# Performance work log

Hardware: AMD Instinct MI355X
Metric: run time of the kernel (lower is better)

## Reference

```python
import jax, jax.numpy as jnp
import numpy as np

H, QP, VP, D, DP = 4, 4, 4, 128, 64
DH = D // H


def setup_inputs() -> dict:
    key = jax.random.key(0)
    ks = jax.random.split(key, 16)
    B, L = 1, 1024
    w_c0 = float(np.log(np.e - 1.0))
    inp = {
        'single': jax.random.normal(ks[0], (B, L, D), jnp.float32),
        'pair': jax.random.normal(ks[1], (B, L, L, DP), jnp.float32),
        'T': jax.random.normal(ks[2], (B, L, 4, 4), jnp.float32),
        'w_C': jnp.full((H,), w_c0, jnp.float32),
        'ln_g': jnp.ones((D,), jnp.float32),
        'ln_b': jnp.zeros((D,), jnp.float32),
        'Wq': jax.random.normal(ks[3], (D, H * DH), jnp.float32) * 0.05,
        'Wk': jax.random.normal(ks[4], (D, H * DH), jnp.float32) * 0.05,
        'Wv': jax.random.normal(ks[5], (D, H * DH), jnp.float32) * 0.05,
        'Wqpt': jax.random.normal(ks[6], (D, H * QP * 3), jnp.float32) * 0.05,
        'Wkpt': jax.random.normal(ks[7], (D, H * QP * 3), jnp.float32) * 0.05,
        'Wvpt': jax.random.normal(ks[8], (D, H * VP * 3), jnp.float32) * 0.05,
        'Wb': jax.random.normal(ks[9], (DP, H), jnp.float32) * 0.05,
        'Wout': jax.random.normal(ks[10], (H * (DH + DP + VP * 3 + VP), D), jnp.float32) * 0.05,
        'b_out': jnp.zeros((D,), jnp.float32),
    }
    return inp


def _layernorm(x, g, b, eps=1e-5):
    x32 = x.astype(jnp.float32)
    mu = x32.mean(-1, keepdims=True)
    var = ((x32 - mu) ** 2).mean(-1, keepdims=True)
    return ((x32 - mu) * jax.lax.rsqrt(var + eps) * g + b).astype(x.dtype)


def reference(single, pair, T, w_C, ln_g, ln_b, Wq, Wk, Wv, Wqpt, Wkpt, Wvpt, Wb, Wout, b_out):
    B, L, Dm = single.shape
    scale_attn = DH ** (-0.5)
    z = _layernorm(single, ln_g, ln_b)
    Q = (z @ Wq).reshape(B, L, H, DH)
    K = (z @ Wk).reshape(B, L, H, DH)
    V = (z @ Wv).reshape(B, L, H, DH)
    Q_pt = (z @ Wqpt).reshape(B, L, H, QP, 3)
    K_pt = (z @ Wkpt).reshape(B, L, H, QP, 3)
    V_pt = (z @ Wvpt).reshape(B, L, H, VP, 3)
    R = T[..., :3, :3]   # [B,L,3,3]
    t = T[..., :3, 3]    # [B,L,3]
    # global-frame points: R @ p + t
    Q_g = jnp.einsum('blxy,blhpy->blhpx', R, Q_pt) + t[:, :, None, None, :]
    K_g = jnp.einsum('blxy,blhpy->blhpx', R, K_pt) + t[:, :, None, None, :]
    V_g = jnp.einsum('blxy,blhpy->blhpx', R, V_pt) + t[:, :, None, None, :]
    # scalar QK score [B,H,L,L]
    s_attn = jnp.einsum('bihd,bjhd->bhij', Q, K) * scale_attn
    # pair bias [B,H,L,L]
    b_attn = jnp.einsum('bijc,ch->bhij', pair, Wb)
    # squared point distance [B,H,L,L]
    diff = Q_g[:, :, None] - K_g[:, None]          # [B,L,L,H,QP,3]
    d2 = jnp.moveaxis((diff ** 2).sum((-1, -2)), -1, 1)
    w_pt = jax.nn.softplus(w_C)[None, :, None, None]
    attn = jax.nn.softmax(s_attn + b_attn - 0.5 * w_pt * d2, axis=-1)
    # scalar values [B,L,H*DH]
    o_s = jnp.einsum('bhij,bjhd->bihd', attn, V).reshape(B, L, H * DH)
    # point values aggregated in global frame then mapped back: R^T (p - t)
    o_pt_g = jnp.einsum('bhij,bjhpx->bihpx', attn, V_g)
    o_pt = jnp.einsum('blyx,blhpy->blhpx', R, o_pt_g - t[:, :, None, None, :])
    o_pt_n = jnp.sqrt((o_pt ** 2).sum(-1))
    # pair aggregation [B,L,H*DP]
    o_pair = jnp.einsum('bhij,bijc->bihc', attn, pair).reshape(B, L, H * DP)
    out = jnp.concatenate([o_s, o_pair, o_pt.reshape(B, L, -1), o_pt_n.reshape(B, L, -1)], axis=-1)
    return single + out @ Wout + b_out
```

## Files before the change

kernel.cpp:

```cpp
#include <hip/hip_runtime.h>
#include <math.h>

#define L_SEQ 1024
#define DM 128
#define JC 32
#define NCH (L_SEQ / JC)

#define OFF_KHAT 0
#define OFF_QHAT (L_SEQ * 192)
#define OFF_V    (OFF_QHAT + L_SEQ * 192)
#define OFF_VG   (OFF_V + L_SEQ * DM)

typedef __attribute__((address_space(1))) const void* gas_t;
typedef __attribute__((address_space(3))) void* las_t;

__device__ __forceinline__ void async16(const float4* g, float4* l) {
    __builtin_amdgcn_global_load_lds((gas_t)g, (las_t)l, 16, 0, 0);
}
#define ASYNC_BAR() asm volatile("s_waitcnt lgkmcnt(0)\n\ts_barrier" ::: "memory")

__global__ __launch_bounds__(256) void ipa_prep(
    const float* __restrict__ single, const float* __restrict__ T,
    const float* __restrict__ w_C, const float* __restrict__ ln_g, const float* __restrict__ ln_b,
    const float* __restrict__ Wq, const float* __restrict__ Wk, const float* __restrict__ Wv,
    const float* __restrict__ Wqpt, const float* __restrict__ Wkpt, const float* __restrict__ Wvpt,
    float* __restrict__ ws)
{
    __shared__ float z_lds[4][128];
    __shared__ float proj[4][528];
    __shared__ float qg[4][4][4][3];
    __shared__ float kg[4][4][4][3];
    __shared__ float cq[4][4], ck[4][4];

    const int t = threadIdx.x;
    const int wv = t >> 6, lane = t & 63;
    const int i0 = blockIdx.x << 2;
    const int i = i0 + wv;

    float x0 = single[i*DM + lane];
    float x1 = single[i*DM + 64 + lane];
    float s = x0 + x1, s2 = x0*x0 + x1*x1;
    #pragma unroll
    for (int off = 1; off < 64; off <<= 1) { s += __shfl_xor(s, off); s2 += __shfl_xor(s2, off); }
    float mu = s * 0.0078125f;
    float var = s2 * 0.0078125f - mu*mu;
    float rs = rsqrtf(var + 1e-5f);
    z_lds[wv][lane]      = (x0 - mu) * rs * ln_g[lane]      + ln_b[lane];
    z_lds[wv][lane + 64] = (x1 - mu) * rs * ln_g[lane + 64] + ln_b[lane + 64];
    __syncthreads();

    for (int cc = t; cc < 528; cc += 256) {
        const float* W; int col, ncol;
        if (cc < 128)      { W = Wq;   col = cc;       ncol = 128; }
        else if (cc < 256) { W = Wk;   col = cc - 128; ncol = 128; }
        else if (cc < 384) { W = Wv;   col = cc - 256; ncol = 128; }
        else if (cc < 432) { W = Wqpt; col = cc - 384; ncol = 48;  }
        else if (cc < 480) { W = Wkpt; col = cc - 432; ncol = 48;  }
        else               { W = Wvpt; col = cc - 480; ncol = 48;  }
        float a0 = 0.f, a1 = 0.f, a2 = 0.f, a3 = 0.f;
        #pragma unroll 8
        for (int k = 0; k < 128; ++k) {
            float w = W[k*ncol + col];
            a0 = fmaf(z_lds[0][k], w, a0);
            a1 = fmaf(z_lds[1][k], w, a1);
            a2 = fmaf(z_lds[2][k], w, a2);
            a3 = fmaf(z_lds[3][k], w, a3);
        }
        proj[0][cc] = a0; proj[1][cc] = a1; proj[2][cc] = a2; proj[3][cc] = a3;
    }
    __syncthreads();

    if (t < 64) {
        int r = t >> 4, h = (t >> 2) & 3, p = t & 3;
        int ii = i0 + r;
        float R[3][3], tt[3];
        #pragma unroll
        for (int x = 0; x < 3; ++x) {
            #pragma unroll
            for (int y = 0; y < 3; ++y) R[x][y] = T[ii*16 + x*4 + y];
            tt[x] = T[ii*16 + x*4 + 3];
        }
        int base = 384 + (h*4 + p)*3;
        float q0 = proj[r][base],    q1 = proj[r][base+1],  q2 = proj[r][base+2];
        float k0 = proj[r][base+48], k1 = proj[r][base+49], k2 = proj[r][base+50];
        float v0 = proj[r][base+96], v1 = proj[r][base+97], v2 = proj[r][base+98];
        #pragma unroll
        for (int x = 0; x < 3; ++x) {
            float qq = R[x][0]*q0 + R[x][1]*q1 + R[x][2]*q2 + tt[x];
            float kk = R[x][0]*k0 + R[x][1]*k1 + R[x][2]*k2 + tt[x];
            float vv = R[x][0]*v0 + R[x][1]*v1 + R[x][2]*v2 + tt[x];
            qg[r][h][p][x] = qq;
            kg[r][h][p][x] = kk;
            ws[OFF_VG + ii*48 + h*12 + p*3 + x] = vv;
        }
    }
    __syncthreads();

    if (t < 32) {
        int r = t >> 3, h = (t >> 1) & 3, isk = t & 1;
        float w = w_C[h];
        float wp = log1pf(__expf(w));
        float sq = 0.f;
        #pragma unroll
        for (int p = 0; p < 4; ++p)
            #pragma unroll
            for (int x = 0; x < 3; ++x) {
                float g = isk ? kg[r][h][p][x] : qg[r][h][p][x];
                sq += g*g;
            }
        float c = -0.5f * wp * sq;
        if (isk) ck[r][h] = c; else cq[r][h] = c;
    }
    __syncthreads();

    for (int idx = t; idx < 512; idx += 256) {
        int r = idx >> 7, d = idx & 127;
        ws[OFF_V + (size_t)(i0 + r)*DM + d] = proj[r][256 + d];
    }
    const float scale_attn = 0.17677669529663687f;
    for (int idx = t; idx < 768; idx += 256) {
        int r = idx / 192, rem = idx % 192;
        int h = rem / 48, k = rem % 48;
        int ii = i0 + r;
        float w = w_C[h];
        float wp = log1pf(__expf(w));
        float kv, qv;
        if (k < 32) {
            kv = proj[r][128 + h*32 + k];
            qv = scale_attn * proj[r][h*32 + k];
        } else if (k < 44) {
            int e = k - 32;
            kv = kg[r][h][e/3][e%3];
            qv = wp * qg[r][h][e/3][e%3];
        } else if (k == 44) { kv = ck[r][h]; qv = 1.0f; }
        else if (k == 45)   { kv = 1.0f;    qv = cq[r][h]; }
        else                { kv = 0.f;     qv = 0.f; }
        ws[OFF_KHAT + (size_t)ii*192 + h*48 + k] = kv;
        ws[OFF_QHAT + (size_t)ii*192 + h*48 + k] = qv;
    }
}

__global__ __launch_bounds__(256, 2) void ipa_attn(
    const float* __restrict__ single, const float* __restrict__ pair,
    const float* __restrict__ T, const float* __restrict__ Wb,
    const float* __restrict__ Wout, const float* __restrict__ b_out,
    const float* __restrict__ ws, float* __restrict__ out)
{
    __shared__ __align__(16) float4 pair_lds[2][2][JC][16];
    __shared__ float bias_part[4][2][JC][5];
    __shared__ float p_lds[4][2][JC];
    __shared__ float alpha_lds[4][2];
    __shared__ float l_lds[4][2];
    __shared__ __align__(16) float4 qhat_lds[2][4][12];
    __shared__ __align__(16) float4 wb_lds[64];
    __shared__ float og_lds[2][4][12];
    __shared__ __align__(16) float u_lds[2][448];

    const int t = threadIdx.x;
    const int wv = t >> 6, lane = t & 63;
    const int i0 = blockIdx.x * 2;

    if (t < 96)       ((float4*)qhat_lds)[t] = ((const float4*)(ws + OFF_QHAT))[(size_t)i0*48 + t];
    else if (t < 160) wb_lds[t - 96] = ((const float4*)Wb)[t - 96];

    const int r_b = lane >> 5, j_b = lane & 31;
    const int r_s = lane & 1,  j_s = lane >> 1;
    const int d4  = lane & 7,  jg_s = lane >> 3;
    const int c4p = lane >> 4, jg_p = lane & 15;
    const int g4  = lane & 3,  jg_g = lane >> 2;
    const int g4c = (g4 < 3) ? g4 : 0;

    float m_run = -INFINITY, l_run = 0.f;
    float4 accp[2][4];
    float4 accs[2];
    float4 accg[2];
    #pragma unroll
    for (int r = 0; r < 2; ++r) {
        accs[r] = make_float4(0.f,0.f,0.f,0.f);
        accg[r] = make_float4(0.f,0.f,0.f,0.f);
        #pragma unroll
        for (int h = 0; h < 4; ++h) accp[r][h] = make_float4(0.f,0.f,0.f,0.f);
    }

    const float4* pair4 = (const float4*)pair;
    const float4* kh4   = (const float4*)(ws + OFF_KHAT);
    const float4* v4    = (const float4*)(ws + OFF_V);
    const float4* vg4   = (const float4*)(ws + OFF_VG);
    float4* plds_flat   = &pair_lds[0][0][0][0];

    {
        #pragma unroll
        for (int it = 0; it < 4; ++it) {
            int idx = it*256 + t;
            int row = idx >> 9, j = (idx >> 4) & 31, slot = idx & 15;
            int c4 = slot ^ (j & 7);
            async16(pair4 + ((size_t)(i0 + row)*L_SEQ + j)*16 + c4, plds_flat + idx);
        }
    }

    for (int ch = 0; ch < NCH; ++ch) {
        const int cur = ch & 1;
        const int j0 = ch * JC;

        ASYNC_BAR();
        if (ch + 1 < NCH) {
            const int jn = (ch + 1) * JC;
            #pragma unroll
            for (int it = 0; it < 4; ++it) {
                int idx = it*256 + t;
                int row = idx >> 9, j = (idx >> 4) & 31, slot = idx & 15;
                int c4 = slot ^ (j & 7);
                async16(pair4 + ((size_t)(i0 + row)*L_SEQ + jn + j)*16 + c4,
                        plds_flat + (1 - cur)*1024 + idx);
            }
            asm volatile("s_waitcnt vmcnt(4)" ::: "memory");
        } else {
            asm volatile("s_waitcnt vmcnt(0)" ::: "memory");
        }
        ASYNC_BAR();

        float4 kh[12];
        {
            const float4* kp = kh4 + (size_t)(j0 + j_s)*48 + wv*12;
            #pragma unroll
            for (int k4 = 0; k4 < 12; ++k4) kh[k4] = kp[k4];
        }
        float4 vv[4];
        #pragma unroll
        for (int jj = 0; jj < 4; ++jj)
            vv[jj] = v4[(size_t)(j0 + jg_s + 8*jj)*32 + wv*8 + d4];
        float4 gvv[2];
        #pragma unroll
        for (int jj = 0; jj < 2; ++jj)
            gvv[jj] = vg4[(size_t)(j0 + jg_g + 16*jj)*12 + wv*3 + g4c];

        {
            float bx=0.f, by=0.f, bz=0.f, bw=0.f;
            #pragma unroll
            for (int cp = 0; cp < 4; ++cp) {
                int c4 = (wv << 2) + cp;
                int sw = c4 ^ (j_b & 7);
                float4 pv = pair_lds[cur][r_b][j_b][sw];
                float4 w0 = wb_lds[c4*4+0], w1 = wb_lds[c4*4+1], w2 = wb_lds[c4*4+2], w3 = wb_lds[c4*4+3];
                bx += pv.x*w0.x + pv.y*w1.x + pv.z*w2.x + pv.w*w3.x;
                by += pv.x*w0.y + pv.y*w1.y + pv.z*w2.y + pv.w*w3.y;
                bz += pv.x*w0.z + pv.y*w1.z + pv.z*w2.z + pv.w*w3.z;
                bw += pv.x*w0.w + pv.y*w1.w + pv.z*w2.w + pv.w*w3.w;
            }
            bias_part[wv][r_b][j_b][0] = bx; bias_part[wv][r_b][j_b][1] = by;
            bias_part[wv][r_b][j_b][2] = bz; bias_part[wv][r_b][j_b][3] = bw;
        }
        ASYNC_BAR();

        {
            float d = 0.f;
            #pragma unroll
            for (int k4 = 0; k4 < 12; ++k4) {
                float4 q = qhat_lds[r_s][wv][k4];
                d = fmaf(kh[k4].x, q.x, d); d = fmaf(kh[k4].y, q.y, d);
                d = fmaf(kh[k4].z, q.z, d); d = fmaf(kh[k4].w, q.w, d);
            }
            float bias = bias_part[0][r_s][j_s][wv] + bias_part[1][r_s][j_s][wv]
                       + bias_part[2][r_s][j_s][wv] + bias_part[3][r_s][j_s][wv];
            float logit = d + bias;
            float cmax = logit;
            #pragma unroll
            for (int off = 2; off < 64; off <<= 1) cmax = fmaxf(cmax, __shfl_xor(cmax, off));
            float mn = fmaxf(m_run, cmax);
            float alpha = __expf(m_run - mn);
            float p = __expf(logit - mn);
            float ps = p;
            #pragma unroll
            for (int off = 2; off < 64; off <<= 1) ps += __shfl_xor(ps, off);
            l_run = l_run * alpha + ps;
            m_run = mn;
            p_lds[wv][r_s][j_s] = p;
            if (j_s == 0) alpha_lds[wv][r_s] = alpha;
        }
        ASYNC_BAR();

        {
            float al[4][2];
            #pragma unroll
            for (int h = 0; h < 4; ++h) { al[h][0] = alpha_lds[h][0]; al[h][1] = alpha_lds[h][1]; }
            #pragma unroll
            for (int r = 0; r < 2; ++r) {
                #pragma unroll
                for (int h = 0; h < 4; ++h) {
                    float a = al[h][r];
                    accp[r][h].x *= a; accp[r][h].y *= a; accp[r][h].z *= a; accp[r][h].w *= a;
                }
                float a = al[wv][r];
                accs[r].x *= a; accs[r].y *= a; accs[r].z *= a; accs[r].w *= a;
                accg[r].x *= a; accg[r].y *= a; accg[r].z *= a; accg[r].w *= a;
            }
            #pragma unroll
            for (int jj = 0; jj < 2; ++jj) {
                int j = jg_p + 16*jj;
                int sw = ((wv << 2) + c4p) ^ (j & 7);
                #pragma unroll
                for (int r = 0; r < 2; ++r) {
                    float4 pv = pair_lds[cur][r][j][sw];
                    float p0 = p_lds[0][r][j], p1 = p_lds[1][r][j];
                    float p2 = p_lds[2][r][j], p3 = p_lds[3][r][j];
                    accp[r][0].x = fmaf(p0, pv.x, accp[r][0].x); accp[r][0].y = fmaf(p0, pv.y, accp[r][0].y);
                    accp[r][0].z = fmaf(p0, pv.z, accp[r][0].z); accp[r][0].w = fmaf(p0, pv.w, accp[r][0].w);
                    accp[r][1].x = fmaf(p1, pv.x, accp[r][1].x); accp[r][1].y = fmaf(p1, pv.y, accp[r][1].y);
                    accp[r][1].z = fmaf(p1, pv.z, accp[r][1].z); accp[r][1].w = fmaf(p1, pv.w, accp[r][1].w);
                    accp[r][2].x = fmaf(p2, pv.x, accp[r][2].x); accp[r][2].y = fmaf(p2, pv.y, accp[r][2].y);
                    accp[r][2].z = fmaf(p2, pv.z, accp[r][2].z); accp[r][2].w = fmaf(p2, pv.w, accp[r][2].w);
                    accp[r][3].x = fmaf(p3, pv.x, accp[r][3].x); accp[r][3].y = fmaf(p3, pv.y, accp[r][3].y);
                    accp[r][3].z = fmaf(p3, pv.z, accp[r][3].z); accp[r][3].w = fmaf(p3, pv.w, accp[r][3].w);
                }
            }
            #pragma unroll
            for (int jj = 0; jj < 4; ++jj) {
                int j = jg_s + 8*jj;
                float pa = p_lds[wv][0][j], pb = p_lds[wv][1][j];
                accs[0].x = fmaf(pa, vv[jj].x, accs[0].x); accs[0].y = fmaf(pa, vv[jj].y, accs[0].y);
                accs[0].z = fmaf(pa, vv[jj].z, accs[0].z); accs[0].w = fmaf(pa, vv[jj].w, accs[0].w);
                accs[1].x = fmaf(pb, vv[jj].x, accs[1].x); accs[1].y = fmaf(pb, vv[jj].y, accs[1].y);
                accs[1].z = fmaf(pb, vv[jj].z, accs[1].z); accs[1].w = fmaf(pb, vv[jj].w, accs[1].w);
            }
            #pragma unroll
            for (int jj = 0; jj < 2; ++jj) {
                int j = jg_g + 16*jj;
                float pa = p_lds[wv][0][j], pb = p_lds[wv][1][j];
                accg[0].x = fmaf(pa, gvv[jj].x, accg[0].x); accg[0].y = fmaf(pa, gvv[jj].y, accg[0].y);
                accg[0].z = fmaf(pa, gvv[jj].z, accg[0].z); accg[0].w = fmaf(pa, gvv[jj].w, accg[0].w);
                accg[1].x = fmaf(pb, gvv[jj].x, accg[1].x); accg[1].y = fmaf(pb, gvv[jj].y, accg[1].y);
                accg[1].z = fmaf(pb, gvv[jj].z, accg[1].z); accg[1].w = fmaf(pb, gvv[jj].w, accg[1].w);
            }
        }
    }

    #pragma unroll
    for (int r = 0; r < 2; ++r) {
        #pragma unroll
        for (int h = 0; h < 4; ++h) {
            #pragma unroll
            for (int off = 1; off < 16; off <<= 1) {
                accp[r][h].x += __shfl_xor(accp[r][h].x, off);
                accp[r][h].y += __shfl_xor(accp[r][h].y, off);
                accp[r][h].z += __shfl_xor(accp[r][h].z, off);
                accp[r][h].w += __shfl_xor(accp[r][h].w, off);
            }
        }
        #pragma unroll
        for (int off = 8; off < 64; off <<= 1) {
            accs[r].x += __shfl_xor(accs[r].x, off); accs[r].y += __shfl_xor(accs[r].y, off);
            accs[r].z += __shfl_xor(accs[r].z, off); accs[r].w += __shfl_xor(accs[r].w, off);
        }
        #pragma unroll
        for (int off = 4; off < 64; off <<= 1) {
            accg[r].x += __shfl_xor(accg[r].x, off); accg[r].y += __shfl_xor(accg[r].y, off);
            accg[r].z += __shfl_xor(accg[r].z, off); accg[r].w += __shfl_xor(accg[r].w, off);
        }
    }
    if (lane < 2) l_lds[wv][lane] = l_run;
    __syncthreads();
    float invl[4][2];
    #pragma unroll
    for (int h = 0; h < 4; ++h) { invl[h][0] = 1.f / l_lds[h][0]; invl[h][1] = 1.f / l_lds[h][1]; }

    if (lane < 8) {
        #pragma unroll
        for (int r = 0; r < 2; ++r) {
            float sc = invl[wv][r];
            int base = wv*32 + lane*4;
            u_lds[r][base+0] = accs[r].x*sc; u_lds[r][base+1] = accs[r].y*sc;
            u_lds[r][base+2] = accs[r].z*sc; u_lds[r][base+3] = accs[r].w*sc;
        }
    }
    if ((lane & 15) == 0) {
        int c4 = wv*4 + (lane >> 4);
        #pragma unroll
        for (int r = 0; r < 2; ++r)
            #pragma unroll
            for (int h = 0; h < 4; ++h) {
                float sc = invl[h][r];
                int base = 128 + h*64 + c4*4;
                u_lds[r][base+0] = accp[r][h].x*sc; u_lds[r][base+1] = accp[r][h].y*sc;
                u_lds[r][base+2] = accp[r][h].z*sc; u_lds[r][base+3] = accp[r][h].w*sc;
            }
    }
    if (lane < 3) {
        #pragma unroll
        for (int r = 0; r < 2; ++r) {
            float sc = invl[wv][r];
            og_lds[r][wv][lane*4+0] = accg[r].x*sc; og_lds[r][wv][lane*4+1] = accg[r].y*sc;
            og_lds[r][wv][lane*4+2] = accg[r].z*sc; og_lds[r][wv][lane*4+3] = accg[r].w*sc;
        }
    }
    __syncthreads();

    if (t < 32) {
        int r = t >> 4, idx = t & 15, h = idx >> 2, p = idx & 3;
        int ii = i0 + r;
        float R[3][3], tt[3];
        #pragma unroll
        for (int x = 0; x < 3; ++x) {
            #pragma unroll
            for (int y = 0; y < 3; ++y) R[x][y] = T[ii*16 + x*4 + y];
            tt[x] = T[ii*16 + x*4 + 3];
        }
        float v0 = og_lds[r][h][p*3+0] - tt[0];
        float v1 = og_lds[r][h][p*3+1] - tt[1];
        float v2 = og_lds[r][h][p*3+2] - tt[2];
        float n2 = 0.f;
        #pragma unroll
        for (int x = 0; x < 3; ++x) {
            float o = R[0][x]*v0 + R[1][x]*v1 + R[2][x]*v2;
            u_lds[r][384 + h*12 + p*3 + x] = o;
            n2 += o*o;
        }
        u_lds[r][432 + h*4 + p] = sqrtf(n2);
    }
    __syncthreads();

    {
        int r = t >> 7, d = t & 127;
        int ii = i0 + r;
        float acc = single[ii*DM + d] + b_out[d];
        const float4* u4 = (const float4*)u_lds[r];
        #pragma unroll 4
        for (int k4 = 0; k4 < 112; ++k4) {
            float4 u = u4[k4];
            const float* wp = Wout + (size_t)(k4*4)*128 + d;
            acc = fmaf(u.x, wp[0],   acc);
            acc = fmaf(u.y, wp[128], acc);
            acc = fmaf(u.z, wp[256], acc);
            acc = fmaf(u.w, wp[384], acc);
        }
        out[ii*DM + d] = acc;
    }
}

extern "C" void kernel_launch(void* const* d_in, const int* in_sizes, int n_in,
                              void* d_out, int out_size, void* d_ws, size_t ws_size,
                              hipStream_t stream)
{
    const float* single = (const float*)d_in[0];
    const float* pair   = (const float*)d_in[1];
    const float* T      = (const float*)d_in[2];
    const float* w_C    = (const float*)d_in[3];
    const float* ln_g   = (const float*)d_in[4];
    const float* ln_b   = (const float*)d_in[5];
    const float* Wq     = (const float*)d_in[6];
    const float* Wk     = (const float*)d_in[7];
    const float* Wv     = (const float*)d_in[8];
    const float* Wqpt   = (const float*)d_in[9];
    const float* Wkpt   = (const float*)d_in[10];
    const float* Wvpt   = (const float*)d_in[11];
    const float* Wb     = (const float*)d_in[12];
    const float* Wout   = (const float*)d_in[13];
    const float* b_out  = (const float*)d_in[14];
    float* out = (float*)d_out;
    float* ws  = (float*)d_ws;

    ipa_prep<<<256, 256, 0, stream>>>(single, T, w_C, ln_g, ln_b, Wq, Wk, Wv, Wqpt, Wkpt, Wvpt, ws);
    ipa_attn<<<512, 256, 0, stream>>>(single, pair, T, Wb, Wout, b_out, ws, out);
}
```

Measured before the change: 473.8 us.

## Restructure attention kernel to one query row per block with 64-key chunks

The attention kernel now processes one query row per block instead of two, launching 1024 blocks with a launch bound allowing 4 blocks per CU. The key chunk is widened from 32 to 64 so each lane owns one key in the softmax step. Key-hat loads are issued before the next pair prefetch, and the pipeline wait is relaxed. The final output projection is split across both halves of the block with a reduction through shared memory. This aims to raise occupancy and parallelism for the pair-streaming loop, but it halves reuse of the loaded K/V data per block and relies on the looser wait ordering being correct.

```diff
diff --git a/kernel.cpp b/kernel.cpp
--- a/kernel.cpp
+++ b/kernel.cpp
@@ -3,7 +3,7 @@
 
 #define L_SEQ 1024
 #define DM 128
-#define JC 32
+#define JC 64
 #define NCH (L_SEQ / JC)
 
 #define OFF_KHAT 0
@@ -18,6 +18,7 @@
     __builtin_amdgcn_global_load_lds((gas_t)g, (las_t)l, 16, 0, 0);
 }
 #define ASYNC_BAR() asm volatile("s_waitcnt lgkmcnt(0)\n\ts_barrier" ::: "memory")
+#define MEMBAR()    asm volatile("" ::: "memory")
 
 __global__ __launch_bounds__(256) void ipa_prep(
     const float* __restrict__ single, const float* __restrict__ T,
@@ -140,300 +141,263 @@
     }
 }
 
-__global__ __launch_bounds__(256, 2) void ipa_attn(
+__global__ __launch_bounds__(256, 4) void ipa_attn(
     const float* __restrict__ single, const float* __restrict__ pair,
     const float* __restrict__ T, const float* __restrict__ Wb,
     const float* __restrict__ Wout, const float* __restrict__ b_out,
     const float* __restrict__ ws, float* __restrict__ out)
 {
-    __shared__ __align__(16) float4 pair_lds[2][2][JC][16];
-    __shared__ float bias_part[4][2][JC][5];
-    __shared__ float p_lds[4][2][JC];
-    __shared__ float alpha_lds[4][2];
-    __shared__ float l_lds[4][2];
-    __shared__ __align__(16) float4 qhat_lds[2][4][12];
-    __shared__ __align__(16) float4 wb_lds[64];
-    __shared__ float og_lds[2][4][12];
-    __shared__ __align__(16) float u_lds[2][448];
+    __shared__ __align__(16) float4 pair_s[2][JC][16];
+    __shared__ float bias_s[16][JC];
+    __shared__ float p_s[4][JC];
+    __shared__ __align__(16) float4 qhat_s[48];
+    __shared__ __align__(16) float4 wb_s[64];
+    __shared__ float l_s[4];
+    __shared__ float alpha_s[4];
 
     const int t = threadIdx.x;
     const int wv = t >> 6, lane = t & 63;
-    const int i0 = blockIdx.x * 2;
-
-    if (t < 96)       ((float4*)qhat_lds)[t] = ((const float4*)(ws + OFF_QHAT))[(size_t)i0*48 + t];
-    else if (t < 160) wb_lds[t - 96] = ((const float4*)Wb)[t - 96];
-
-    const int r_b = lane >> 5, j_b = lane & 31;
-    const int r_s = lane & 1,  j_s = lane >> 1;
-    const int d4  = lane & 7,  jg_s = lane >> 3;
-    const int c4p = lane >> 4, jg_p = lane & 15;
-    const int g4  = lane & 3,  jg_g = lane >> 2;
-    const int g4c = (g4 < 3) ? g4 : 0;
+    const int i = blockIdx.x;
+
+    if (t < 48)       qhat_s[t]    = ((const float4*)(ws + OFF_QHAT))[(size_t)i*48 + t];
+    else if (t < 112) wb_s[t - 48] = ((const float4*)Wb)[t - 48];
+    MEMBAR();
 
     float m_run = -INFINITY, l_run = 0.f;
-    float4 accp[2][4];
-    float4 accs[2];
-    float4 accg[2];
-    #pragma unroll
-    for (int r = 0; r < 2; ++r) {
-        accs[r] = make_float4(0.f,0.f,0.f,0.f);
-        accg[r] = make_float4(0.f,0.f,0.f,0.f);
-        #pragma unroll
-        for (int h = 0; h < 4; ++h) accp[r][h] = make_float4(0.f,0.f,0.f,0.f);
-    }
+    float4 accp[4], accs, accg;
+    accs = make_float4(0.f,0.f,0.f,0.f);
+    accg = make_float4(0.f,0.f,0.f,0.f);
+    #pragma unroll
+    for (int h = 0; h < 4; ++h) accp[h] = make_float4(0.f,0.f,0.f,0.f);
 
     const float4* pair4 = (const float4*)pair;
     const float4* kh4   = (const float4*)(ws + OFF_KHAT);
     const float4* v4    = (const float4*)(ws + OFF_V);
     const float4* vg4   = (const float4*)(ws + OFF_VG);
-    float4* plds_flat   = &pair_lds[0][0][0][0];
-
-    {
-        #pragma unroll
-        for (int it = 0; it < 4; ++it) {
-            int idx = it*256 + t;
-            int row = idx >> 9, j = (idx >> 4) & 31, slot = idx & 15;
-            int c4 = slot ^ (j & 7);
-            async16(pair4 + ((size_t)(i0 + row)*L_SEQ + j)*16 + c4, plds_flat + idx);
-        }
+    float4* pbase = &pair_s[0][0][0];
+
+    const int d4  = lane & 7,  jg7 = lane >> 3;
+    const int c4p = lane >> 4, jgp = lane & 15;
+    const int g4  = lane & 3,  jg4 = lane >> 2;
+    const int g4c = (g4 < 3) ? g4 : 0;
+
+    #pragma unroll
+    for (int it = 0; it < 4; ++it) {
+        int idx = it*256 + t;
+        int j = idx >> 4, slot = idx & 15;
+        async16(pair4 + ((size_t)i*L_SEQ + j)*16 + (slot ^ (j & 7)), pbase + idx);
     }
 
     for (int ch = 0; ch < NCH; ++ch) {
         const int cur = ch & 1;
-        const int j0 = ch * JC;
+        const int j0  = ch * JC;
 
         ASYNC_BAR();
+
+        float4 khr[12];
+        {
+            const float4* kp = kh4 + (size_t)(j0 + lane)*48 + wv*12;
+            #pragma unroll
+            for (int k4 = 0; k4 < 12; ++k4) khr[k4] = kp[k4];
+        }
+        MEMBAR();
         if (ch + 1 < NCH) {
-            const int jn = (ch + 1) * JC;
+            const int jn = j0 + JC;
             #pragma unroll
             for (int it = 0; it < 4; ++it) {
                 int idx = it*256 + t;
-                int row = idx >> 9, j = (idx >> 4) & 31, slot = idx & 15;
-                int c4 = slot ^ (j & 7);
-                async16(pair4 + ((size_t)(i0 + row)*L_SEQ + jn + j)*16 + c4,
-                        plds_flat + (1 - cur)*1024 + idx);
-            }
-            asm volatile("s_waitcnt vmcnt(4)" ::: "memory");
-        } else {
-            asm volatile("s_waitcnt vmcnt(0)" ::: "memory");
-        }
+                int j = idx >> 4, slot = idx & 15;
+                async16(pair4 + ((size_t)i*L_SEQ + jn + j)*16 + (slot ^ (j & 7)),
+                        pbase + (1 - cur)*1024 + idx);
+            }
+        }
+        if (ch == 0)
+            asm volatile("s_waitcnt vmcnt(16)" ::: "memory");
         ASYNC_BAR();
 
-        float4 kh[12];
         {
-            const float4* kp = kh4 + (size_t)(j0 + j_s)*48 + wv*12;
-            #pragma unroll
-            for (int k4 = 0; k4 < 12; ++k4) kh[k4] = kp[k4];
-        }
-        float4 vv[4];
-        #pragma unroll
-        for (int jj = 0; jj < 4; ++jj)
-            vv[jj] = v4[(size_t)(j0 + jg_s + 8*jj)*32 + wv*8 + d4];
-        float4 gvv[2];
-        #pragma unroll
-        for (int jj = 0; jj < 2; ++jj)
-            gvv[jj] = vg4[(size_t)(j0 + jg_g + 16*jj)*12 + wv*3 + g4c];
-
-        {
-            float bx=0.f, by=0.f, bz=0.f, bw=0.f;
-            #pragma unroll
-            for (int cp = 0; cp < 4; ++cp) {
-                int c4 = (wv << 2) + cp;
-                int sw = c4 ^ (j_b & 7);
-                float4 pv = pair_lds[cur][r_b][j_b][sw];
-                float4 w0 = wb_lds[c4*4+0], w1 = wb_lds[c4*4+1], w2 = wb_lds[c4*4+2], w3 = wb_lds[c4*4+3];
-                bx += pv.x*w0.x + pv.y*w1.x + pv.z*w2.x + pv.w*w3.x;
-                by += pv.x*w0.y + pv.y*w1.y + pv.z*w2.y + pv.w*w3.y;
-                bz += pv.x*w0.z + pv.y*w1.z + pv.z*w2.z + pv.w*w3.z;
-                bw += pv.x*w0.w + pv.y*w1.w + pv.z*w2.w + pv.w*w3.w;
-            }
-            bias_part[wv][r_b][j_b][0] = bx; bias_part[wv][r_b][j_b][1] = by;
-            bias_part[wv][r_b][j_b][2] = bz; bias_part[wv][r_b][j_b][3] = bw;
+            float b0=0.f, b1=0.f, b2=0.f, b3=0.f;
+            #pragma unroll
+            for (int k = 0; k < 4; ++k) {
+                float4 pv = pair_s[cur][lane][(wv*4 + k) ^ (lane & 7)];
+                float4 w0 = wb_s[wv*16 + k*4 + 0], w1 = wb_s[wv*16 + k*4 + 1];
+                float4 w2 = wb_s[wv*16 + k*4 + 2], w3 = wb_s[wv*16 + k*4 + 3];
+                b0 += pv.x*w0.x + pv.y*w1.x + pv.z*w2.x + pv.w*w3.x;
+                b1 += pv.x*w0.y + pv.y*w1.y + pv.z*w2.y + pv.w*w3.y;
+                b2 += pv.x*w0.z + pv.y*w1.z + pv.z*w2.z + pv.w*w3.z;
+                b3 += pv.x*w0.w + pv.y*w1.w + pv.z*w2.w + pv.w*w3.w;
+            }
+            bias_s[wv*4 + 0][lane] = b0; bias_s[wv*4 + 1][lane] = b1;
+            bias_s[wv*4 + 2][lane] = b2; bias_s[wv*4 + 3][lane] = b3;
         }
         ASYNC_BAR();
 
+        float my_alpha;
         {
             float d = 0.f;
             #pragma unroll
             for (int k4 = 0; k4 < 12; ++k4) {
-                float4 q = qhat_lds[r_s][wv][k4];
-                d = fmaf(kh[k4].x, q.x, d); d = fmaf(kh[k4].y, q.y, d);
-                d = fmaf(kh[k4].z, q.z, d); d = fmaf(kh[k4].w, q.w, d);
-            }
-            float bias = bias_part[0][r_s][j_s][wv] + bias_part[1][r_s][j_s][wv]
-                       + bias_part[2][r_s][j_s][wv] + bias_part[3][r_s][j_s][wv];
+                float4 q = qhat_s[wv*12 + k4];
+                d = fmaf(khr[k4].x, q.x, d); d = fmaf(khr[k4].y, q.y, d);
+                d = fmaf(khr[k4].z, q.z, d); d = fmaf(khr[k4].w, q.w, d);
+            }
+            float bias = bias_s[0*4 + wv][lane] + bias_s[1*4 + wv][lane]
+                       + bias_s[2*4 + wv][lane] + bias_s[3*4 + wv][lane];
             float logit = d + bias;
             float cmax = logit;
             #pragma unroll
-            for (int off = 2; off < 64; off <<= 1) cmax = fmaxf(cmax, __shfl_xor(cmax, off));
+            for (int off = 1; off < 64; off <<= 1) cmax = fmaxf(cmax, __shfl_xor(cmax, off));
             float mn = fmaxf(m_run, cmax);
-            float alpha = __expf(m_run - mn);
-            float p = __expf(logit - mn);
-            float ps = p;
-            #pragma unroll
-            for (int off = 2; off < 64; off <<= 1) ps += __shfl_xor(ps, off);
-            l_run = l_run * alpha + ps;
+            my_alpha = __expf(m_run - mn);
+            float pj = __expf(logit - mn);
+            float ps = pj;
+            #pragma unroll
+            for (int off = 1; off < 64; off <<= 1) ps += __shfl_xor(ps, off);
+            l_run = l_run * my_alpha + ps;
             m_run = mn;
-            p_lds[wv][r_s][j_s] = p;
-            if (j_s == 0) alpha_lds[wv][r_s] = alpha;
+            p_s[wv][lane] = pj;
+            if (lane == 0) alpha_s[wv] = my_alpha;
         }
         ASYNC_BAR();
 
         {
-            float al[4][2];
-            #pragma unroll
-            for (int h = 0; h < 4; ++h) { al[h][0] = alpha_lds[h][0]; al[h][1] = alpha_lds[h][1]; }
-            #pragma unroll
-            for (int r = 0; r < 2; ++r) {
-                #pragma unroll
-                for (int h = 0; h < 4; ++h) {
-                    float a = al[h][r];
-                    accp[r][h].x *= a; accp[r][h].y *= a; accp[r][h].z *= a; accp[r][h].w *= a;
-                }
-                float a = al[wv][r];
-                accs[r].x *= a; accs[r].y *= a; accs[r].z *= a; accs[r].w *= a;
-                accg[r].x *= a; accg[r].y *= a; accg[r].z *= a; accg[r].w *= a;
-            }
-            #pragma unroll
-            for (int jj = 0; jj < 2; ++jj) {
-                int j = jg_p + 16*jj;
-                int sw = ((wv << 2) + c4p) ^ (j & 7);
-                #pragma unroll
-                for (int r = 0; r < 2; ++r) {
-                    float4 pv = pair_lds[cur][r][j][sw];
-                    float p0 = p_lds[0][r][j], p1 = p_lds[1][r][j];
-                    float p2 = p_lds[2][r][j], p3 = p_lds[3][r][j];
-                    accp[r][0].x = fmaf(p0, pv.x, accp[r][0].x); accp[r][0].y = fmaf(p0, pv.y, accp[r][0].y);
-                    accp[r][0].z = fmaf(p0, pv.z, accp[r][0].z); accp[r][0].w = fmaf(p0, pv.w, accp[r][0].w);
-                    accp[r][1].x = fmaf(p1, pv.x, accp[r][1].x); accp[r][1].y = fmaf(p1, pv.y, accp[r][1].y);
-                    accp[r][1].z = fmaf(p1, pv.z, accp[r][1].z); accp[r][1].w = fmaf(p1, pv.w, accp[r][1].w);
-                    accp[r][2].x = fmaf(p2, pv.x, accp[r][2].x); accp[r][2].y = fmaf(p2, pv.y, accp[r][2].y);
-                    accp[r][2].z = fmaf(p2, pv.z, accp[r][2].z); accp[r][2].w = fmaf(p2, pv.w, accp[r][2].w);
-                    accp[r][3].x = fmaf(p3, pv.x, accp[r][3].x); accp[r][3].y = fmaf(p3, pv.y, accp[r][3].y);
-                    accp[r][3].z = fmaf(p3, pv.z, accp[r][3].z); accp[r][3].w = fmaf(p3, pv.w, accp[r][3].w);
-                }
-            }
+            float4 vvr[8];
+            #pragma unroll
+            for (int jj = 0; jj < 8; ++jj)
+                vvr[jj] = v4[(size_t)(j0 + jg7 + 8*jj)*32 + wv*8 + d4];
+            float4 gvr[4];
+            #pragma unroll
+            for (int jj = 0; jj < 4; ++jj)
+                gvr[jj] = vg4[(size_t)(j0 + jg4 + 16*jj)*12 + wv*3 + g4c];
+
+            float a0 = alpha_s[0], a1 = alpha_s[1], a2 = alpha_s[2], a3 = alpha_s[3];
+            accp[0].x *= a0; accp[0].y *= a0; accp[0].z *= a0; accp[0].w *= a0;
+            accp[1].x *= a1; accp[1].y *= a1; accp[1].z *= a1; accp[1].w *= a1;
+            accp[2].x *= a2; accp[2].y *= a2; accp[2].z *= a2; accp[2].w *= a2;
+            accp[3].x *= a3; accp[3].y *= a3; accp[3].z *= a3; accp[3].w *= a3;
+            accs.x *= my_alpha; accs.y *= my_alpha; accs.z *= my_alpha; accs.w *= my_alpha;
+            accg.x *= my_alpha; accg.y *= my_alpha; accg.z *= my_alpha; accg.w *= my_alpha;
+
+            const int c4 = wv*4 + c4p;
             #pragma unroll
             for (int jj = 0; jj < 4; ++jj) {
-                int j = jg_s + 8*jj;
-                float pa = p_lds[wv][0][j], pb = p_lds[wv][1][j];
-                accs[0].x = fmaf(pa, vv[jj].x, accs[0].x); accs[0].y = fmaf(pa, vv[jj].y, accs[0].y);
-                accs[0].z = fmaf(pa, vv[jj].z, accs[0].z); accs[0].w = fmaf(pa, vv[jj].w, accs[0].w);
-                accs[1].x = fmaf(pb, vv[jj].x, accs[1].x); accs[1].y = fmaf(pb, vv[jj].y, accs[1].y);
-                accs[1].z = fmaf(pb, vv[jj].z, accs[1].z); accs[1].w = fmaf(pb, vv[jj].w, accs[1].w);
-            }
-            #pragma unroll
-            for (int jj = 0; jj < 2; ++jj) {
-                int j = jg_g + 16*jj;
-                float pa = p_lds[wv][0][j], pb = p_lds[wv][1][j];
-                accg[0].x = fmaf(pa, gvv[jj].x, accg[0].x); accg[0].y = fmaf(pa, gvv[jj].y, accg[0].y);
-                accg[0].z = fmaf(pa, gvv[jj].z, accg[0].z); accg[0].w = fmaf(pa, gvv[jj].w, accg[0].w);
-                accg[1].x = fmaf(pb, gvv[jj].x, accg[1].x); accg[1].y = fmaf(pb, gvv[jj].y, accg[1].y);
-                accg[1].z = fmaf(pb, gvv[jj].z, accg[1].z); accg[1].w = fmaf(pb, gvv[jj].w, accg[1].w);
-            }
-        }
-    }
-
-    #pragma unroll
-    for (int r = 0; r < 2; ++r) {
-        #pragma unroll
-        for (int h = 0; h < 4; ++h) {
-            #pragma unroll
-            for (int off = 1; off < 16; off <<= 1) {
-                accp[r][h].x += __shfl_xor(accp[r][h].x, off);
-                accp[r][h].y += __shfl_xor(accp[r][h].y, off);
-                accp[r][h].z += __shfl_xor(accp[r][h].z, off);
-                accp[r][h].w += __shfl_xor(accp[r][h].w, off);
-            }
-        }
-        #pragma unroll
-        for (int off = 8; off < 64; off <<= 1) {
-            accs[r].x += __shfl_xor(accs[r].x, off); accs[r].y += __shfl_xor(accs[r].y, off);
-            accs[r].z += __shfl_xor(accs[r].z, off); accs[r].w += __shfl_xor(accs[r].w, off);
-        }
-        #pragma unroll
-        for (int off = 4; off < 64; off <<= 1) {
-            accg[r].x += __shfl_xor(accg[r].x, off); accg[r].y += __shfl_xor(accg[r].y, off);
-            accg[r].z += __shfl_xor(accg[r].z, off); accg[r].w += __shfl_xor(accg[r].w, off);
-        }
-    }
-    if (lane < 2) l_lds[wv][lane] = l_run;
-    __syncthreads();
-    float invl[4][2];
-    #pragma unroll
-    for (int h = 0; h < 4; ++h) { invl[h][0] = 1.f / l_lds[h][0]; invl[h][1] = 1.f / l_lds[h][1]; }
+                int j = jgp + 16*jj;
+                float4 pv = pair_s[cur][j][c4 ^ (j & 7)];
+                float p0 = p_s[0][j], p1 = p_s[1][j], p2 = p_s[2][j], p3 = p_s[3][j];
+                accp[0].x = fmaf(p0, pv.x, accp[0].x); accp[0].y = fmaf(p0, pv.y, accp[0].y);
+                accp[0].z = fmaf(p0, pv.z, accp[0].z); accp[0].w = fmaf(p0, pv.w, accp[0].w);
+                accp[1].x = fmaf(p1, pv.x, accp[1].x); accp[1].y = fmaf(p1, pv.y, accp[1].y);
+                accp[1].z = fmaf(p1, pv.z, accp[1].z); accp[1].w = fmaf(p1, pv.w, accp[1].w);
+                accp[2].x = fmaf(p2, pv.x, accp[2].x); accp[2].y = fmaf(p2, pv.y, accp[2].y);
+                accp[2].z = fmaf(p2, pv.z, accp[2].z); accp[2].w = fmaf(p2, pv.w, accp[2].w);
+                accp[3].x = fmaf(p3, pv.x, accp[3].x); accp[3].y = fmaf(p3, pv.y, accp[3].y);
+                accp[3].z = fmaf(p3, pv.z, accp[3].z); accp[3].w = fmaf(p3, pv.w, accp[3].w);
+            }
+            #pragma unroll
+            for (int jj = 0; jj < 8; ++jj) {
+                int j = jg7 + 8*jj;
+                float pw = p_s[wv][j];
+                accs.x = fmaf(pw, vvr[jj].x, accs.x); accs.y = fmaf(pw, vvr[jj].y, accs.y);
+                accs.z = fmaf(pw, vvr[jj].z, accs.z); accs.w = fmaf(pw, vvr[jj].w, accs.w);
+            }
+            #pragma unroll
+            for (int jj = 0; jj < 4; ++jj) {
+                int j = jg4 + 16*jj;
+                float pw = p_s[wv][j];
+                accg.x = fmaf(pw, gvr[jj].x, accg.x); accg.y = fmaf(pw, gvr[jj].y, accg.y);
+                accg.z = fmaf(pw, gvr[jj].z, accg.z); accg.w = fmaf(pw, gvr[jj].w, accg.w);
+            }
+        }
+    }
+
+    #pragma unroll
+    for (int h = 0; h < 4; ++h) {
+        #pragma unroll
+        for (int off = 1; off < 16; off <<= 1) {
+            accp[h].x += __shfl_xor(accp[h].x, off);
+            accp[h].y += __shfl_xor(accp[h].y, off);
+            accp[h].z += __shfl_xor(accp[h].z, off);
+            accp[h].w += __shfl_xor(accp[h].w, off);
+        }
+    }
+    #pragma unroll
+    for (int off = 8; off < 64; off <<= 1) {
+        accs.x += __shfl_xor(accs.x, off); accs.y += __shfl_xor(accs.y, off);
+        accs.z += __shfl_xor(accs.z, off); accs.w += __shfl_xor(accs.w, off);
+    }
+    #pragma unroll
+    for (int off = 4; off < 64; off <<= 1) {
+        accg.x += __shfl_xor(accg.x, off); accg.y += __shfl_xor(accg.y, off);
+        accg.z += __shfl_xor(accg.z, off); accg.w += __shfl_xor(accg.w, off);
+    }
+    if (lane == 0) l_s[wv] = l_run;
+    __syncthreads();
+
+    float* u    = (float*)pair_s;
+    float* psum = u + 512;
+    float* og   = u + 1024;
+    const float invw = 1.f / l_run;
 
     if (lane < 8) {
-        #pragma unroll
-        for (int r = 0; r < 2; ++r) {
-            float sc = invl[wv][r];
-            int base = wv*32 + lane*4;
-            u_lds[r][base+0] = accs[r].x*sc; u_lds[r][base+1] = accs[r].y*sc;
-            u_lds[r][base+2] = accs[r].z*sc; u_lds[r][base+3] = accs[r].w*sc;
-        }
-    }
-    if ((lane & 15) == 0) {
-        int c4 = wv*4 + (lane >> 4);
-        #pragma unroll
-        for (int r = 0; r < 2; ++r)
-            #pragma unroll
-            for (int h = 0; h < 4; ++h) {
-                float sc = invl[h][r];
-                int base = 128 + h*64 + c4*4;
-                u_lds[r][base+0] = accp[r][h].x*sc; u_lds[r][base+1] = accp[r][h].y*sc;
-                u_lds[r][base+2] = accp[r][h].z*sc; u_lds[r][base+3] = accp[r][h].w*sc;
-            }
+        int base = wv*32 + lane*4;
+        u[base+0] = accs.x*invw; u[base+1] = accs.y*invw;
+        u[base+2] = accs.z*invw; u[base+3] = accs.w*invw;
+    }
+    if (jgp == 0) {
+        int c4 = wv*4 + c4p;
+        float il0 = 1.f/l_s[0], il1 = 1.f/l_s[1], il2 = 1.f/l_s[2], il3 = 1.f/l_s[3];
+        int b0 = 128 + 0*64 + c4*4, b1 = 128 + 1*64 + c4*4, b2 = 128 + 2*64 + c4*4, b3 = 128 + 3*64 + c4*4;
+        u[b0+0] = accp[0].x*il0; u[b0+1] = accp[0].y*il0; u[b0+2] = accp[0].z*il0; u[b0+3] = accp[0].w*il0;
+        u[b1+0] = accp[1].x*il1; u[b1+1] = accp[1].y*il1; u[b1+2] = accp[1].z*il1; u[b1+3] = accp[1].w*il1;
+        u[b2+0] = accp[2].x*il2; u[b2+1] = accp[2].y*il2; u[b2+2] = accp[2].z*il2; u[b2+3] = accp[2].w*il2;
+        u[b3+0] = accp[3].x*il3; u[b3+1] = accp[3].y*il3; u[b3+2] = accp[3].z*il3; u[b3+3] = accp[3].w*il3;
     }
     if (lane < 3) {
-        #pragma unroll
-        for (int r = 0; r < 2; ++r) {
-            float sc = invl[wv][r];
-            og_lds[r][wv][lane*4+0] = accg[r].x*sc; og_lds[r][wv][lane*4+1] = accg[r].y*sc;
-            og_lds[r][wv][lane*4+2] = accg[r].z*sc; og_lds[r][wv][lane*4+3] = accg[r].w*sc;
-        }
-    }
-    __syncthreads();
-
-    if (t < 32) {
-        int r = t >> 4, idx = t & 15, h = idx >> 2, p = idx & 3;
-        int ii = i0 + r;
+        og[wv*12 + lane*4 + 0] = accg.x*invw; og[wv*12 + lane*4 + 1] = accg.y*invw;
+        og[wv*12 + lane*4 + 2] = accg.z*invw; og[wv*12 + lane*4 + 3] = accg.w*invw;
+    }
+    __syncthreads();
+
+    if (t < 16) {
+        int h = t >> 2, p = t & 3;
         float R[3][3], tt[3];
         #pragma unroll
         for (int x = 0; x < 3; ++x) {
             #pragma unroll
-            for (int y = 0; y < 3; ++y) R[x][y] = T[ii*16 + x*4 + y];
-            tt[x] = T[ii*16 + x*4 + 3];
-        }
-        float v0 = og_lds[r][h][p*3+0] - tt[0];
-        float v1 = og_lds[r][h][p*3+1] - tt[1];
-        float v2 = og_lds[r][h][p*3+2] - tt[2];
+            for (int y = 0; y < 3; ++y) R[x][y] = T[i*16 + x*4 + y];
+            tt[x] = T[i*16 + x*4 + 3];
+        }
+        float v0 = og[h*12 + p*3 + 0] - tt[0];
+        float v1 = og[h*12 + p*3 + 1] - tt[1];
+        float v2 = og[h*12 + p*3 + 2] - tt[2];
         float n2 = 0.f;
         #pragma unroll
         for (int x = 0; x < 3; ++x) {
             float o = R[0][x]*v0 + R[1][x]*v1 + R[2][x]*v2;
-            u_lds[r][384 + h*12 + p*3 + x] = o;
+            u[384 + h*12 + p*3 + x] = o;
             n2 += o*o;
         }
-        u_lds[r][432 + h*4 + p] = sqrtf(n2);
+        u[432 + h*4 + p] = sqrtf(n2);
     }
     __syncthreads();
 
     {
-        int r = t >> 7, d = t & 127;
-        int ii = i0 + r;
-        float acc = single[ii*DM + d] + b_out[d];
-        const float4* u4 = (const float4*)u_lds[r];
+        int part = t >> 7, d = t & 127;
+        float acc = part ? 0.f : (single[i*DM + d] + b_out[d]);
+        const float4* u4 = (const float4*)u;
         #pragma unroll 4
-        for (int k4 = 0; k4 < 112; ++k4) {
-            float4 u = u4[k4];
+        for (int k4 = part*56; k4 < part*56 + 56; ++k4) {
+            float4 uv = u4[k4];
             const float* wp = Wout + (size_t)(k4*4)*128 + d;
-            acc = fmaf(u.x, wp[0],   acc);
-            acc = fmaf(u.y, wp[128], acc);
-            acc = fmaf(u.z, wp[256], acc);
-            acc = fmaf(u.w, wp[384], acc);
-        }
-        out[ii*DM + d] = acc;
-    }
+            acc = fmaf(uv.x, wp[0],   acc);
+            acc = fmaf(uv.y, wp[128], acc);
+            acc = fmaf(uv.z, wp[256], acc);
+            acc = fmaf(uv.w, wp[384], acc);
+        }
+        psum[part*128 + d] = acc;
+    }
+    __syncthreads();
+    if (t < 128) out[i*DM + t] = psum[t] + psum[128 + t];
 }
 
 extern "C" void kernel_launch(void* const* d_in, const int* in_sizes, int n_in,
@@ -459,5 +423,5 @@
     float* ws  = (float*)d_ws;
 
     ipa_prep<<<256, 256, 0, stream>>>(single, T, w_C, ln_g, ln_b, Wq, Wk, Wv, Wqpt, Wkpt, Wvpt, ws);
-    ipa_attn<<<512, 256, 0, stream>>>(single, pair, T, Wb, Wout, b_out, ws, out);
+    ipa_attn<<<1024, 256, 0, stream>>>(single, pair, T, Wb, Wout, b_out, ws, out);
 }
```

After: 579.3 us. 1.22x slower.
